# Optimization experiments

Measured on AMD Instinct MI355X. Metric: run time of the kernel, lower is better.

## Reference

```python
import jax, jax.numpy as jnp
import numpy as np

HEADS = 16
EPS = 1e-6


def setup_inputs() -> dict:
    key = jax.random.key(0)
    k1, k2, k3 = jax.random.split(key, 3)
    B, N, C = 4, 4096, 1024
    x = jax.random.normal(k1, (B, N, C), dtype=jnp.float32)
    w_qkv = jax.random.normal(k2, (3 * C, C), dtype=jnp.float32) * (C ** -0.5)
    w_out = jax.random.normal(k3, (C, C), dtype=jnp.float32) * (C ** -0.5)
    b_out = jnp.zeros((C,), dtype=jnp.float32)
    return {"x": x, "w_qkv": w_qkv, "w_out": w_out, "b_out": b_out}


def reference(x, w_qkv, w_out, b_out):
    B, N, C = x.shape
    H = HEADS
    D = C // H
    scale = D ** -0.25

    qkv = x @ w_qkv.T  # [B, N, 3C]
    q, k, v = jnp.split(qkv, 3, axis=-1)

    def heads(t):  # [B, N, C] -> [B, H, N, D]
        return t.reshape(B, N, H, D).transpose(0, 2, 1, 3)

    q, k, v = heads(q), heads(k), heads(v)

    feat = lambda t: jax.nn.elu(t) + 1.0
    q = feat(q) * scale
    k = feat(k) * scale

    kv = jnp.einsum('bhnd,bhne->bhde', k, v)      # [B, H, D, D]
    out = jnp.einsum('bhnd,bhde->bhne', q, kv)    # [B, H, N, D]
    k_sum = k.sum(axis=2)                          # [B, H, D]
    denom = jnp.einsum('bhnd,bhd->bhn', q, k_sum)  # [B, H, N]
    out = out / (denom[..., None] + EPS)

    out = out.transpose(0, 2, 1, 3).reshape(B, N, C)
    return out @ w_out.T + b_out
```

## Files before the change

kernel.cpp:

```cpp
#include <hip/hip_runtime.h>
#include <hip/hip_bf16.h>
#include <cmath>


typedef __bf16 bf16_t;
typedef __attribute__((ext_vector_type(8))) __bf16 bf16x8;
typedef __attribute__((ext_vector_type(4))) __bf16 bf16x4;
typedef __attribute__((ext_vector_type(4))) float f32x4;
typedef __attribute__((ext_vector_type(8))) float f32x8;

#define MFMA16(a, b, c) __builtin_amdgcn_mfma_f32_16x16x32_bf16((a), (b), (c), 0, 0, 0)

#define LDS_PITCH 72

__device__ __forceinline__ f32x4 zf4() { f32x4 z; z[0] = 0.f; z[1] = 0.f; z[2] = 0.f; z[3] = 0.f; return z; }

__device__ __forceinline__ float feat(float x) { return x > 0.f ? x + 1.f : expf(x); }

__device__ __forceinline__ void gld_lds16(const bf16_t* src, bf16_t* dst)
{
    __builtin_amdgcn_global_load_lds(
        (__attribute__((address_space(1))) void*)const_cast<bf16_t*>(src),
        (__attribute__((address_space(3))) void*)dst, 16, 0, 0);
}

template <int NR>
__device__ __forceinline__ void stage_async(const bf16_t* g, int ld, bf16_t* lds, int tid)
{
    const int w = tid >> 6, l = tid & 63;
    constexpr int CALLS = NR >> 5;
#pragma unroll
    for (int p = 0; p < CALLS; ++p) {
        const int chunk = w * CALLS + p;
        const int gidx = chunk * 64 + l;
        const int row = gidx >> 3;
        const int cp = gidx & 7;
        const int c = cp ^ (row & 7);
        gld_lds16(g + row * ld + c * 8, lds + chunk * 512);
    }
}

__device__ __forceinline__ bf16x8 read_frag_sw(const bf16_t* lds, int row, int cg)
{
    const int sw = cg ^ (row & 7);
    return *(const bf16x8*)(lds + row * 64 + sw * 8);
}

template <int NR>
__device__ __forceinline__ void stage_bf16(const bf16_t* g, int ld, bf16_t* lds, int tid)
{
#pragma unroll
    for (int p = 0; p < NR * 8 / 256; ++p) {
        const int gidx = p * 256 + tid;
        const int row = gidx >> 3;
        const int cp = gidx & 7;
        *(bf16x8*)(lds + row * LDS_PITCH + cp * 8) = *(const bf16x8*)(g + row * ld + cp * 8);
    }
}

__device__ __forceinline__ bf16x8 read_frag(const bf16_t* lds, int row, int cg)
{
    return *(const bf16x8*)(lds + row * LDS_PITCH + cg * 8);
}

__global__ __launch_bounds__(256) void cvt_kernel(const float* __restrict__ src, bf16_t* __restrict__ dst)
{
    const size_t idx = ((size_t)blockIdx.x * 256 + threadIdx.x) * 8;
    f32x8 f = *(const f32x8*)(src + idx);
    bf16x8 v;
#pragma unroll
    for (int t = 0; t < 8; ++t) v[t] = (bf16_t)f[t];
    *(bf16x8*)(dst + idx) = v;
}

template <int MODE>
__global__ __launch_bounds__(256, 3) void gemm_bt_kernel(
    const bf16_t* __restrict__ A, const bf16_t* __restrict__ B, int K,
    void* __restrict__ out0, bf16_t* __restrict__ out1, bf16_t* __restrict__ out2,
    const float* __restrict__ bias)
{
    __shared__ __align__(16) bf16_t As[128 * 64];
    __shared__ __align__(16) bf16_t Bs[128 * 64];
    const int tid = threadIdx.x;
    const int l = tid & 63, w = tid >> 6;
    const int wm = w >> 1, wn = w & 1;
    const int quad = l >> 4, r16 = l & 15;
    const int m0 = blockIdx.y * 128;
    const int n0 = blockIdx.x * 128;

    f32x4 acc[4][4];
#pragma unroll
    for (int i = 0; i < 4; ++i)
#pragma unroll
        for (int j = 0; j < 4; ++j) acc[i][j] = zf4();

    const bf16_t* Ab = A + (size_t)m0 * K;
    const bf16_t* Bb = B + (size_t)n0 * K;

    for (int k0 = 0; k0 < K; k0 += 64) {
        stage_async<128>(Ab + k0, K, As, tid);
        stage_async<128>(Bb + k0, K, Bs, tid);
        __syncthreads();
#pragma unroll
        for (int ks = 0; ks < 2; ++ks) {
            const int cg = ks * 4 + quad;
            bf16x8 af[4], bfr[4];
#pragma unroll
            for (int i = 0; i < 4; ++i) af[i] = read_frag_sw(As, wm * 64 + i * 16 + r16, cg);
#pragma unroll
            for (int j = 0; j < 4; ++j) bfr[j] = read_frag_sw(Bs, wn * 64 + j * 16 + r16, cg);
#pragma unroll
            for (int i = 0; i < 4; ++i)
#pragma unroll
                for (int j = 0; j < 4; ++j)
                    acc[i][j] = MFMA16(af[i], bfr[j], acc[i][j]);
        }
        __syncthreads();
    }

    const float scale = 0.3535533905932738f;
#pragma unroll
    for (int i = 0; i < 4; ++i) {
        const int mbase = m0 + wm * 64 + i * 16 + quad * 4;
#pragma unroll
        for (int j = 0; j < 4; ++j) {
            const int col = n0 + wn * 64 + j * 16 + r16;
            if (MODE == 1) {
                float* yp = (float*)out0;
                const float bb = bias[col];
#pragma unroll
                for (int r = 0; r < 4; ++r)
                    yp[(size_t)(mbase + r) * 1024 + col] = acc[i][j][r] + bb;
            } else {
                const int part = col >> 10;
                const int cc = col & 1023;
                const int hh = (mbase >> 12) * 16 + (cc >> 6);
                const int d = cc & 63;
                const int ntok = mbase & 4095;
                if (part == 0) {
                    bf16_t* qp = (bf16_t*)out0 + ((size_t)hh * 4096 + ntok) * 64 + d;
#pragma unroll
                    for (int r = 0; r < 4; ++r)
                        qp[(size_t)r * 64] = (bf16_t)(feat(acc[i][j][r]) * scale);
                } else {
                    bf16_t* tp = (part == 1 ? out1 : out2) + ((size_t)hh * 64 + d) * 4096 + ntok;
                    bf16x4 pk;
#pragma unroll
                    for (int r = 0; r < 4; ++r) {
                        float v = acc[i][j][r];
                        if (part == 1) v = feat(v) * scale;
                        pk[r] = (bf16_t)v;
                    }
                    *(bf16x4*)tp = pk;
                }
            }
        }
    }
}

__global__ __launch_bounds__(256, 2) void kv_partial_kernel(
    const bf16_t* __restrict__ KT, const bf16_t* __restrict__ VT,
    float* __restrict__ kvp, float* __restrict__ ksp_out)
{
    __shared__ __align__(16) bf16_t Ks[64 * LDS_PITCH];
    __shared__ __align__(16) bf16_t Vs[64 * LDS_PITCH];
    const int tid = threadIdx.x;
    const int l = tid & 63, w = tid >> 6;
    const int quad = l >> 4, r16 = l & 15;
    const int hh = blockIdx.x;
    const int ksp = blockIdx.y;
    const bf16_t* kb = KT + (size_t)hh * 64 * 4096 + ksp * 1024;
    const bf16_t* vb = VT + (size_t)hh * 64 * 4096 + ksp * 1024;

    bf16x8 ones;
#pragma unroll
    for (int t = 0; t < 8; ++t) ones[t] = (bf16_t)1.0f;

    f32x4 acc[4], accks[4];
#pragma unroll
    for (int j = 0; j < 4; ++j) { acc[j] = zf4(); accks[j] = zf4(); }

    for (int k0 = 0; k0 < 1024; k0 += 64) {
        stage_bf16<64>(kb + k0, 4096, Ks, tid);
        stage_bf16<64>(vb + k0, 4096, Vs, tid);
        __syncthreads();
#pragma unroll
        for (int ks = 0; ks < 2; ++ks) {
            const int cg = ks * 4 + quad;
            bf16x8 af = read_frag(Vs, w * 16 + r16, cg);
            bf16x8 bk[4];
#pragma unroll
            for (int j = 0; j < 4; ++j) bk[j] = read_frag(Ks, j * 16 + r16, cg);
#pragma unroll
            for (int j = 0; j < 4; ++j) acc[j] = MFMA16(af, bk[j], acc[j]);
            if (w == 0) {
#pragma unroll
                for (int j = 0; j < 4; ++j) accks[j] = MFMA16(ones, bk[j], accks[j]);
            }
        }
        __syncthreads();
    }

    float* ob = kvp + (size_t)(hh * 4 + ksp) * 4096;
    const int ebase = w * 16 + quad * 4;
#pragma unroll
    for (int j = 0; j < 4; ++j)
#pragma unroll
        for (int r = 0; r < 4; ++r)
            ob[(ebase + r) * 64 + j * 16 + r16] = acc[j][r];

    if (w == 0 && quad == 0) {
        float* kso = ksp_out + (size_t)(hh * 4 + ksp) * 64;
#pragma unroll
        for (int j = 0; j < 4; ++j) kso[j * 16 + r16] = accks[j][0];
    }
}

__global__ __launch_bounds__(256) void kvfix_kernel(
    const float* __restrict__ kvp, const float* __restrict__ ksp,
    bf16_t* __restrict__ kvb, bf16_t* __restrict__ ksumb)
{
    const int hh = blockIdx.x, t = threadIdx.x;
    const float* base = kvp + (size_t)hh * 4 * 4096;
    const int off = t * 16;
    bf16x8 o[2];
#pragma unroll
    for (int c = 0; c < 4; ++c) {
        f32x4 s = *(const f32x4*)(base + off + c * 4);
        s += *(const f32x4*)(base + 4096 + off + c * 4);
        s += *(const f32x4*)(base + 8192 + off + c * 4);
        s += *(const f32x4*)(base + 12288 + off + c * 4);
#pragma unroll
        for (int r = 0; r < 4; ++r) o[c >> 1][(c & 1) * 4 + r] = (bf16_t)s[r];
    }
    *(bf16x8*)(kvb + (size_t)hh * 4096 + off) = o[0];
    *(bf16x8*)(kvb + (size_t)hh * 4096 + off + 8) = o[1];
    if (t < 64) {
        const float* kb = ksp + (size_t)hh * 4 * 64;
        ksumb[(size_t)hh * 64 + t] = (bf16_t)(kb[t] + kb[64 + t] + kb[128 + t] + kb[192 + t]);
    }
}

__global__ __launch_bounds__(256, 2) void attn_out_kernel(
    const bf16_t* __restrict__ Q, const bf16_t* __restrict__ kvb, const bf16_t* __restrict__ ksumb,
    bf16_t* __restrict__ att)
{
    __shared__ __align__(16) bf16_t kvT[64 * LDS_PITCH];
    __shared__ __align__(16) bf16_t ksb[64];
    const int tid = threadIdx.x;
    const int l = tid & 63, w = tid >> 6;
    const int quad = l >> 4, r16 = l & 15;
    const int hh = blockIdx.x;
    const int b = hh >> 4, h = hh & 15;
    const int mt = blockIdx.y;

    {
        const int e = tid >> 2, d0 = (tid & 3) * 16;
        const bf16_t* kvbh = kvb + (size_t)hh * 4096;
        *(bf16x8*)(kvT + e * LDS_PITCH + d0)     = *(const bf16x8*)(kvbh + e * 64 + d0);
        *(bf16x8*)(kvT + e * LDS_PITCH + d0 + 8) = *(const bf16x8*)(kvbh + e * 64 + d0 + 8);
        if (tid < 64) ksb[tid] = ksumb[(size_t)hh * 64 + tid];
    }
    __syncthreads();

    f32x4 acc[4][4];
    f32x4 dacc[4];
#pragma unroll
    for (int i = 0; i < 4; ++i) {
        dacc[i] = zf4();
#pragma unroll
        for (int j = 0; j < 4; ++j) acc[i][j] = zf4();
    }

    const int m0w = mt * 256 + w * 64;
    const bf16_t* qb = Q + (size_t)hh * 4096 * 64;
#pragma unroll
    for (int ks = 0; ks < 2; ++ks) {
        bf16x8 kf = *(const bf16x8*)(ksb + ks * 32 + quad * 8);
        if (r16 != 0) {
#pragma unroll
            for (int t = 0; t < 8; ++t) kf[t] = (bf16_t)0.f;
        }
        bf16x8 bfr[4];
#pragma unroll
        for (int j = 0; j < 4; ++j)
            bfr[j] = *(const bf16x8*)(kvT + (j * 16 + r16) * LDS_PITCH + ks * 32 + quad * 8);
#pragma unroll
        for (int i = 0; i < 4; ++i) {
            const bf16_t* qp = qb + (size_t)(m0w + i * 16 + r16) * 64 + ks * 32 + quad * 8;
            const bf16x8 af = *(const bf16x8*)qp;
            dacc[i] = MFMA16(af, kf, dacc[i]);
#pragma unroll
            for (int j = 0; j < 4; ++j) acc[i][j] = MFMA16(af, bfr[j], acc[i][j]);
        }
    }

#pragma unroll
    for (int i = 0; i < 4; ++i) {
        float den[4];
#pragma unroll
        for (int r = 0; r < 4; ++r)
            den[r] = __shfl(dacc[i][r], l & 48) + 1e-6f;
#pragma unroll
        for (int j = 0; j < 4; ++j) {
            const size_t colb = (size_t)h * 64 + j * 16 + r16;
#pragma unroll
            for (int r = 0; r < 4; ++r) {
                const int ntok = m0w + i * 16 + quad * 4 + r;
                att[((size_t)b * 4096 + ntok) * 1024 + colb] = (bf16_t)(acc[i][j][r] / den[r]);
            }
        }
    }
}

extern "C" void kernel_launch(void* const* d_in, const int* in_sizes, int n_in,
                              void* d_out, int out_size, void* d_ws, size_t ws_size,
                              hipStream_t stream)
{
    const float* x    = (const float*)d_in[0];
    const float* wqkv = (const float*)d_in[1];
    const float* wout = (const float*)d_in[2];
    const float* bout = (const float*)d_in[3];
    float* y = (float*)d_out;

    char* ws = (char*)d_ws;
    bf16_t* xb    = (bf16_t*)ws;
    bf16_t* wqkvb = (bf16_t*)(ws + (size_t)32 * 1048576);
    bf16_t* woutb = (bf16_t*)(ws + (size_t)38 * 1048576);
    bf16_t* Q     = (bf16_t*)(ws + (size_t)40 * 1048576);
    bf16_t* KT    = (bf16_t*)(ws + (size_t)72 * 1048576);
    bf16_t* VT    = (bf16_t*)(ws + (size_t)104 * 1048576);
    float* kvp    = (float*)ws;
    float* ksp    = (float*)(ws + (size_t)4 * 1048576);
    bf16_t* kvb   = (bf16_t*)(ws + (size_t)5 * 1048576);
    bf16_t* ksumb = (bf16_t*)(ws + (size_t)6 * 1048576);
    bf16_t* att   = KT;

    cvt_kernel<<<8192, 256, 0, stream>>>(x, xb);
    cvt_kernel<<<1536, 256, 0, stream>>>(wqkv, wqkvb);
    cvt_kernel<<<512, 256, 0, stream>>>(wout, woutb);

    gemm_bt_kernel<0><<<dim3(24, 128), 256, 0, stream>>>(xb, wqkvb, 1024, Q, KT, VT, nullptr);
    kv_partial_kernel<<<dim3(64, 4), 256, 0, stream>>>(KT, VT, kvp, ksp);
    kvfix_kernel<<<64, 256, 0, stream>>>(kvp, ksp, kvb, ksumb);
    attn_out_kernel<<<dim3(64, 16), 256, 0, stream>>>(Q, kvb, ksumb, att);
    gemm_bt_kernel<1><<<dim3(8, 128), 256, 0, stream>>>(att, woutb, 1024, y, nullptr, nullptr, bout);
}
```

Before: 332.6 us.

## Use 256x256 tiles with double-buffered async LDS pipeline in GEMM kernel

Both GEMMs move from a 128x128 tile with 4 waves to a 256x256 tile with 8 waves and 128 KB of double-buffered LDS. Global-to-LDS async loads for future K-tiles are split into regions and issued between MFMA phases, with explicit vmcnt waits, barriers and setprio so loads overlap compute. The aim is more data reuse per block and hiding memory latency. In exchange it uses more registers and LDS, allows fewer blocks per CU, and launches fewer blocks (256 for the output GEMM), so the last wave of blocks may leave CUs idle.

```diff
diff --git a/kernel.cpp b/kernel.cpp
--- a/kernel.cpp
+++ b/kernel.cpp
@@ -24,26 +24,31 @@
         (__attribute__((address_space(3))) void*)dst, 16, 0, 0);
 }
 
-template <int NR>
-__device__ __forceinline__ void stage_async(const bf16_t* g, int ld, bf16_t* lds, int tid)
+template <int R>
+__device__ __forceinline__ void stage_region(const bf16_t* Ab, const bf16_t* Bb, int K,
+                                             int koff, bf16_t* buf, int tid)
 {
     const int w = tid >> 6, l = tid & 63;
-    constexpr int CALLS = NR >> 5;
-#pragma unroll
-    for (int p = 0; p < CALLS; ++p) {
-        const int chunk = w * CALLS + p;
+    bf16_t* dst = buf + R * 8192;
+#pragma unroll
+    for (int p = 0; p < 2; ++p) {
+        const int chunk = w * 2 + p;
         const int gidx = chunk * 64 + l;
-        const int row = gidx >> 3;
-        const int cp = gidx & 7;
-        const int c = cp ^ (row & 7);
-        gld_lds16(g + row * ld + c * 8, lds + chunk * 512);
-    }
-}
-
-__device__ __forceinline__ bf16x8 read_frag_sw(const bf16_t* lds, int row, int cg)
-{
-    const int sw = cg ^ (row & 7);
-    return *(const bf16x8*)(lds + row * 64 + sw * 8);
+        const int rr = gidx >> 3;
+        const int c = (gidx & 7) ^ (rr & 7);
+        const bf16_t* src;
+        if (R == 0)      src = Bb + (size_t)rr * K;
+        else if (R == 1) src = Bb + (size_t)(128 + rr) * K;
+        else if (R == 2) src = Ab + (size_t)(rr + (rr & 64)) * K;
+        else             src = Ab + (size_t)(64 + rr + (rr & 64)) * K;
+        gld_lds16(src + koff + c * 8, dst + chunk * 512);
+    }
+}
+
+__device__ __forceinline__ bf16x8 rfrag(const bf16_t* region, int rr, int cg)
+{
+    const int sw = cg ^ (rr & 7);
+    return *(const bf16x8*)(region + rr * 64 + sw * 8);
 }
 
 template <int NR>
@@ -74,54 +79,118 @@
 }
 
 template <int MODE>
-__global__ __launch_bounds__(256, 3) void gemm_bt_kernel(
+__global__ __launch_bounds__(512, 2) void gemm_bt_kernel(
     const bf16_t* __restrict__ A, const bf16_t* __restrict__ B, int K,
     void* __restrict__ out0, bf16_t* __restrict__ out1, bf16_t* __restrict__ out2,
     const float* __restrict__ bias)
 {
-    __shared__ __align__(16) bf16_t As[128 * 64];
-    __shared__ __align__(16) bf16_t Bs[128 * 64];
+    __shared__ __align__(16) bf16_t lds[2 * 32768];
     const int tid = threadIdx.x;
     const int l = tid & 63, w = tid >> 6;
-    const int wm = w >> 1, wn = w & 1;
+    const int wm = w >> 2, wn = w & 3;
     const int quad = l >> 4, r16 = l & 15;
-    const int m0 = blockIdx.y * 128;
-    const int n0 = blockIdx.x * 128;
-
-    f32x4 acc[4][4];
-#pragma unroll
-    for (int i = 0; i < 4; ++i)
-#pragma unroll
-        for (int j = 0; j < 4; ++j) acc[i][j] = zf4();
+    const int m0 = blockIdx.y * 256;
+    const int n0 = blockIdx.x * 256;
+    const int NT = K >> 6;
 
     const bf16_t* Ab = A + (size_t)m0 * K;
     const bf16_t* Bb = B + (size_t)n0 * K;
 
-    for (int k0 = 0; k0 < K; k0 += 64) {
-        stage_async<128>(Ab + k0, K, As, tid);
-        stage_async<128>(Bb + k0, K, Bs, tid);
-        __syncthreads();
-#pragma unroll
-        for (int ks = 0; ks < 2; ++ks) {
-            const int cg = ks * 4 + quad;
-            bf16x8 af[4], bfr[4];
-#pragma unroll
-            for (int i = 0; i < 4; ++i) af[i] = read_frag_sw(As, wm * 64 + i * 16 + r16, cg);
-#pragma unroll
-            for (int j = 0; j < 4; ++j) bfr[j] = read_frag_sw(Bs, wn * 64 + j * 16 + r16, cg);
-#pragma unroll
-            for (int i = 0; i < 4; ++i)
+    f32x4 acc[8][4];
+#pragma unroll
+    for (int i = 0; i < 8; ++i)
+#pragma unroll
+        for (int j = 0; j < 4; ++j) acc[i][j] = zf4();
+
+    stage_region<0>(Ab, Bb, K, 0, lds, tid);
+    stage_region<1>(Ab, Bb, K, 0, lds, tid);
+    stage_region<2>(Ab, Bb, K, 0, lds, tid);
+    stage_region<3>(Ab, Bb, K, 0, lds, tid);
+    stage_region<0>(Ab, Bb, K, 64, lds + 32768, tid);
+    stage_region<1>(Ab, Bb, K, 64, lds + 32768, tid);
+    stage_region<2>(Ab, Bb, K, 64, lds + 32768, tid);
+    asm volatile("s_waitcnt vmcnt(6)" ::: "memory");
+    __builtin_amdgcn_sched_barrier(0);
+    __builtin_amdgcn_s_barrier();
+
+    for (int t = 0; t < NT; ++t) {
+        bf16_t* cb = lds + (t & 1) * 32768;
+        bf16_t* nb = lds + ((t & 1) ^ 1) * 32768;
+
+        bf16x8 bfr[4][2], af[2][2];
+
+        const bf16_t* breg = cb + (wn >> 1) * 8192;
+#pragma unroll
+        for (int j = 0; j < 4; ++j) {
+            const int rr = (wn & 1) * 64 + j * 16 + r16;
+            bfr[j][0] = rfrag(breg, rr, quad);
+            bfr[j][1] = rfrag(breg, rr, 4 + quad);
+        }
+#pragma unroll
+        for (int i2 = 0; i2 < 2; ++i2) {
+            const int rr = wm * 64 + i2 * 16 + r16;
+            af[i2][0] = rfrag(cb + 2 * 8192, rr, quad);
+            af[i2][1] = rfrag(cb + 2 * 8192, rr, 4 + quad);
+        }
+        if (t + 1 < NT) stage_region<3>(Ab, Bb, K, (t + 1) * 64, nb, tid);
+        __builtin_amdgcn_s_barrier();
+        asm volatile("s_waitcnt lgkmcnt(0)" ::: "memory");
+        __builtin_amdgcn_sched_barrier(0);
+        __builtin_amdgcn_s_setprio(1);
+#pragma unroll
+        for (int ks = 0; ks < 2; ++ks)
+#pragma unroll
+            for (int i2 = 0; i2 < 2; ++i2)
 #pragma unroll
                 for (int j = 0; j < 4; ++j)
-                    acc[i][j] = MFMA16(af[i], bfr[j], acc[i][j]);
-        }
-        __syncthreads();
+                    acc[i2][j] = MFMA16(af[i2][ks], bfr[j][ks], acc[i2][j]);
+        __builtin_amdgcn_s_setprio(0);
+        __builtin_amdgcn_s_barrier();
+
+#pragma unroll
+        for (int ph = 1; ph < 4; ++ph) {
+            const int mb = ph * 2;
+#pragma unroll
+            for (int i2 = 0; i2 < 2; ++i2) {
+                const int i = mb + i2;
+                const bf16_t* areg = cb + (size_t)(2 + (i >> 2)) * 8192;
+                const int rr = wm * 64 + (i & 3) * 16 + r16;
+                af[i2][0] = rfrag(areg, rr, quad);
+                af[i2][1] = rfrag(areg, rr, 4 + quad);
+            }
+            if (t + 2 < NT) {
+                if (ph == 1) stage_region<0>(Ab, Bb, K, (t + 2) * 64, cb, tid);
+                if (ph == 2) stage_region<1>(Ab, Bb, K, (t + 2) * 64, cb, tid);
+                if (ph == 3) stage_region<2>(Ab, Bb, K, (t + 2) * 64, cb, tid);
+            }
+            if (ph == 3) {
+                if (t + 2 < NT) {
+                    asm volatile("s_waitcnt vmcnt(6)" ::: "memory");
+                } else if (t + 2 == NT) {
+                    asm volatile("s_waitcnt vmcnt(0)" ::: "memory");
+                }
+                __builtin_amdgcn_sched_barrier(0);
+            }
+            __builtin_amdgcn_s_barrier();
+            asm volatile("s_waitcnt lgkmcnt(0)" ::: "memory");
+            __builtin_amdgcn_sched_barrier(0);
+            __builtin_amdgcn_s_setprio(1);
+#pragma unroll
+            for (int ks = 0; ks < 2; ++ks)
+#pragma unroll
+                for (int i2 = 0; i2 < 2; ++i2)
+#pragma unroll
+                    for (int j = 0; j < 4; ++j)
+                        acc[mb + i2][j] = MFMA16(af[i2][ks], bfr[j][ks], acc[mb + i2][j]);
+            __builtin_amdgcn_s_setprio(0);
+            __builtin_amdgcn_s_barrier();
+        }
     }
 
     const float scale = 0.3535533905932738f;
 #pragma unroll
-    for (int i = 0; i < 4; ++i) {
-        const int mbase = m0 + wm * 64 + i * 16 + quad * 4;
+    for (int i = 0; i < 8; ++i) {
+        const int mbase = m0 + wm * 128 + i * 16 + quad * 4;
 #pragma unroll
         for (int j = 0; j < 4; ++j) {
             const int col = n0 + wn * 64 + j * 16 + r16;
@@ -340,9 +409,9 @@
     cvt_kernel<<<1536, 256, 0, stream>>>(wqkv, wqkvb);
     cvt_kernel<<<512, 256, 0, stream>>>(wout, woutb);
 
-    gemm_bt_kernel<0><<<dim3(24, 128), 256, 0, stream>>>(xb, wqkvb, 1024, Q, KT, VT, nullptr);
+    gemm_bt_kernel<0><<<dim3(12, 64), 512, 0, stream>>>(xb, wqkvb, 1024, Q, KT, VT, nullptr);
     kv_partial_kernel<<<dim3(64, 4), 256, 0, stream>>>(KT, VT, kvp, ksp);
     kvfix_kernel<<<64, 256, 0, stream>>>(kvp, ksp, kvb, ksumb);
     attn_out_kernel<<<dim3(64, 16), 256, 0, stream>>>(Q, kvb, ksumb, att);
-    gemm_bt_kernel<1><<<dim3(8, 128), 256, 0, stream>>>(att, woutb, 1024, y, nullptr, nullptr, bout);
-}
+    gemm_bt_kernel<1><<<dim3(4, 64), 512, 0, stream>>>(att, woutb, 1024, y, nullptr, nullptr, bout);
+}
```

After: 333.2 us. No clear change (+0.2%).

## Rewrite GEMM as 256x256 tile, 8-wave, double-buffered ping-pong pipeline

Applied to the files above, without the earlier changes.

Replaces the 128x128, 4-wave GEMM with a 256x256 tile computed by 8 waves. Each wave now owns 128x64 of output. K-panels are double-buffered in LDS through async global-to-LDS loads, with fine-grained vmcnt waits, barriers and s_setprio so loads overlap the MFMA bursts. The aim is more data reuse per loaded byte and hidden global latency. In exchange it uses 128KB of LDS, more accumulator registers per wave, and fewer blocks: 768 and 256 tiles across 256 CUs.

```diff
diff --git a/kernel.cpp b/kernel.cpp
--- a/kernel.cpp
+++ b/kernel.cpp
@@ -24,26 +24,34 @@
         (__attribute__((address_space(3))) void*)dst, 16, 0, 0);
 }
 
-template <int NR>
-__device__ __forceinline__ void stage_async(const bf16_t* g, int ld, bf16_t* lds, int tid)
+template <int RT>
+__device__ __forceinline__ const bf16_t* panel_src(const bf16_t* Ab, const bf16_t* Bb, int K, int rr)
+{
+    if (RT == 0) return Bb + (size_t)rr * K;
+    if (RT == 1) return Bb + (size_t)(128 + rr) * K;
+    if (RT == 2) return Ab + (size_t)(rr + (rr & 64)) * K;
+    return Ab + (size_t)(64 + rr + (rr & 64)) * K;
+}
+
+template <int RT>
+__device__ __forceinline__ void stage_panel(const bf16_t* Ab, const bf16_t* Bb, int K,
+                                            int koff, bf16_t* dst, int tid)
 {
     const int w = tid >> 6, l = tid & 63;
-    constexpr int CALLS = NR >> 5;
-#pragma unroll
-    for (int p = 0; p < CALLS; ++p) {
-        const int chunk = w * CALLS + p;
+#pragma unroll
+    for (int p = 0; p < 2; ++p) {
+        const int chunk = w * 2 + p;
         const int gidx = chunk * 64 + l;
-        const int row = gidx >> 3;
-        const int cp = gidx & 7;
-        const int c = cp ^ (row & 7);
-        gld_lds16(g + row * ld + c * 8, lds + chunk * 512);
-    }
-}
-
-__device__ __forceinline__ bf16x8 read_frag_sw(const bf16_t* lds, int row, int cg)
-{
-    const int sw = cg ^ (row & 7);
-    return *(const bf16x8*)(lds + row * 64 + sw * 8);
+        const int rr = gidx >> 3;
+        const int c = (gidx & 7) ^ (rr & 7);
+        gld_lds16(panel_src<RT>(Ab, Bb, K, rr) + koff + c * 8, dst + chunk * 512);
+    }
+}
+
+__device__ __forceinline__ bf16x8 rfrag(const bf16_t* panel, int rr, int cg)
+{
+    const int sw = cg ^ (rr & 7);
+    return *(const bf16x8*)(panel + rr * 64 + sw * 8);
 }
 
 template <int NR>
@@ -73,55 +81,117 @@
     *(bf16x8*)(dst + idx) = v;
 }
 
+#define GBAR() __builtin_amdgcn_s_barrier()
+#define WAITL() do { asm volatile("s_waitcnt lgkmcnt(0)" ::: "memory"); \
+                     __builtin_amdgcn_sched_barrier(0); } while (0)
+#define VMC6() do { asm volatile("s_waitcnt vmcnt(6)" ::: "memory"); \
+                    __builtin_amdgcn_sched_barrier(0); } while (0)
+#define VMC0() do { asm volatile("s_waitcnt vmcnt(0)" ::: "memory"); \
+                    __builtin_amdgcn_sched_barrier(0); } while (0)
+
 template <int MODE>
-__global__ __launch_bounds__(256, 3) void gemm_bt_kernel(
+__global__ __launch_bounds__(512, 2) void gemm_bt_kernel(
     const bf16_t* __restrict__ A, const bf16_t* __restrict__ B, int K,
     void* __restrict__ out0, bf16_t* __restrict__ out1, bf16_t* __restrict__ out2,
     const float* __restrict__ bias)
 {
-    __shared__ __align__(16) bf16_t As[128 * 64];
-    __shared__ __align__(16) bf16_t Bs[128 * 64];
+    __shared__ __align__(16) bf16_t B0a[8192], B0b[8192], A0a[8192], A0b[8192];
+    __shared__ __align__(16) bf16_t B1a[8192], B1b[8192], A1a[8192], A1b[8192];
     const int tid = threadIdx.x;
     const int l = tid & 63, w = tid >> 6;
-    const int wm = w >> 1, wn = w & 1;
+    const int wm = w >> 2, wn = w & 3;
     const int quad = l >> 4, r16 = l & 15;
-    const int m0 = blockIdx.y * 128;
-    const int n0 = blockIdx.x * 128;
-
-    f32x4 acc[4][4];
-#pragma unroll
-    for (int i = 0; i < 4; ++i)
-#pragma unroll
-        for (int j = 0; j < 4; ++j) acc[i][j] = zf4();
+    const int m0 = blockIdx.y * 256;
+    const int n0 = blockIdx.x * 256;
+    const int NT = K >> 6;
 
     const bf16_t* Ab = A + (size_t)m0 * K;
     const bf16_t* Bb = B + (size_t)n0 * K;
 
-    for (int k0 = 0; k0 < K; k0 += 64) {
-        stage_async<128>(Ab + k0, K, As, tid);
-        stage_async<128>(Bb + k0, K, Bs, tid);
-        __syncthreads();
-#pragma unroll
-        for (int ks = 0; ks < 2; ++ks) {
-            const int cg = ks * 4 + quad;
-            bf16x8 af[4], bfr[4];
-#pragma unroll
-            for (int i = 0; i < 4; ++i) af[i] = read_frag_sw(As, wm * 64 + i * 16 + r16, cg);
-#pragma unroll
-            for (int j = 0; j < 4; ++j) bfr[j] = read_frag_sw(Bs, wn * 64 + j * 16 + r16, cg);
-#pragma unroll
-            for (int i = 0; i < 4; ++i)
+    f32x4 acc[8][4];
+#pragma unroll
+    for (int i = 0; i < 8; ++i)
+#pragma unroll
+        for (int j = 0; j < 4; ++j) acc[i][j] = zf4();
+
+    bf16x8 bfr[4][2], af[2][2];
+
+    auto loadB = [&](const bf16_t* Blo, const bf16_t* Bhi) {
+        const bf16_t* breg = (wn & 2) ? Bhi : Blo;
+#pragma unroll
+        for (int j = 0; j < 4; ++j) {
+            const int rr = (wn & 1) * 64 + j * 16 + r16;
+            bfr[j][0] = rfrag(breg, rr, quad);
+            bfr[j][1] = rfrag(breg, rr, 4 + quad);
+        }
+    };
+    auto loadA = [&](const bf16_t* areg, int fr) {
+#pragma unroll
+        for (int i2 = 0; i2 < 2; ++i2) {
+            const int rr = wm * 64 + (fr + i2) * 16 + r16;
+            af[i2][0] = rfrag(areg, rr, quad);
+            af[i2][1] = rfrag(areg, rr, 4 + quad);
+        }
+    };
+    auto mfma8 = [&](int mb) {
+        __builtin_amdgcn_s_setprio(1);
+#pragma unroll
+        for (int ks = 0; ks < 2; ++ks)
+#pragma unroll
+            for (int i2 = 0; i2 < 2; ++i2)
 #pragma unroll
                 for (int j = 0; j < 4; ++j)
-                    acc[i][j] = MFMA16(af[i], bfr[j], acc[i][j]);
-        }
-        __syncthreads();
+                    acc[mb + i2][j] = MFMA16(af[i2][ks], bfr[j][ks], acc[mb + i2][j]);
+        __builtin_amdgcn_s_setprio(0);
+    };
+
+    stage_panel<0>(Ab, Bb, K, 0, B0a, tid);
+    stage_panel<1>(Ab, Bb, K, 0, B0b, tid);
+    stage_panel<2>(Ab, Bb, K, 0, A0a, tid);
+    stage_panel<3>(Ab, Bb, K, 0, A0b, tid);
+    stage_panel<0>(Ab, Bb, K, 64, B1a, tid);
+    stage_panel<1>(Ab, Bb, K, 64, B1b, tid);
+    stage_panel<2>(Ab, Bb, K, 64, A1a, tid);
+    VMC6();
+    GBAR();
+
+    for (int t = 0; t < NT; t += 2) {
+        const int k2 = (t + 2) * 64, k3 = (t + 3) * 64;
+        const bool p2 = (t + 2) < NT, p3 = (t + 3) < NT;
+
+        loadB(B0a, B0b); loadA(A0a, 0);
+        stage_panel<3>(Ab, Bb, K, (t + 1) * 64, A1b, tid);
+        GBAR(); WAITL(); mfma8(0); GBAR();
+        loadA(A0a, 2);
+        if (p2) stage_panel<0>(Ab, Bb, K, k2, B0a, tid);
+        GBAR(); WAITL(); mfma8(2); GBAR();
+        loadA(A0b, 0);
+        if (p2) stage_panel<1>(Ab, Bb, K, k2, B0b, tid);
+        GBAR(); WAITL(); mfma8(4); GBAR();
+        loadA(A0b, 2);
+        if (p2) { stage_panel<2>(Ab, Bb, K, k2, A0a, tid); VMC6(); }
+        else    { VMC0(); }
+        GBAR(); WAITL(); mfma8(6); GBAR();
+
+        loadB(B1a, B1b); loadA(A1a, 0);
+        if (p2) stage_panel<3>(Ab, Bb, K, k2, A0b, tid);
+        GBAR(); WAITL(); mfma8(0); GBAR();
+        loadA(A1a, 2);
+        if (p3) stage_panel<0>(Ab, Bb, K, k3, B1a, tid);
+        GBAR(); WAITL(); mfma8(2); GBAR();
+        loadA(A1b, 0);
+        if (p3) stage_panel<1>(Ab, Bb, K, k3, B1b, tid);
+        GBAR(); WAITL(); mfma8(4); GBAR();
+        loadA(A1b, 2);
+        if (p3) { stage_panel<2>(Ab, Bb, K, k3, A1a, tid); VMC6(); }
+        else    { VMC0(); }
+        GBAR(); WAITL(); mfma8(6); GBAR();
     }
 
     const float scale = 0.3535533905932738f;
 #pragma unroll
-    for (int i = 0; i < 4; ++i) {
-        const int mbase = m0 + wm * 64 + i * 16 + quad * 4;
+    for (int i = 0; i < 8; ++i) {
+        const int mbase = m0 + wm * 128 + i * 16 + quad * 4;
 #pragma unroll
         for (int j = 0; j < 4; ++j) {
             const int col = n0 + wn * 64 + j * 16 + r16;
@@ -340,9 +410,9 @@
     cvt_kernel<<<1536, 256, 0, stream>>>(wqkv, wqkvb);
     cvt_kernel<<<512, 256, 0, stream>>>(wout, woutb);
 
-    gemm_bt_kernel<0><<<dim3(24, 128), 256, 0, stream>>>(xb, wqkvb, 1024, Q, KT, VT, nullptr);
+    gemm_bt_kernel<0><<<dim3(12, 64), 512, 0, stream>>>(xb, wqkvb, 1024, Q, KT, VT, nullptr);
     kv_partial_kernel<<<dim3(64, 4), 256, 0, stream>>>(KT, VT, kvp, ksp);
     kvfix_kernel<<<64, 256, 0, stream>>>(kvp, ksp, kvb, ksumb);
     attn_out_kernel<<<dim3(64, 16), 256, 0, stream>>>(Q, kvb, ksumb, att);
-    gemm_bt_kernel<1><<<dim3(8, 128), 256, 0, stream>>>(att, woutb, 1024, y, nullptr, nullptr, bout);
-}
+    gemm_bt_kernel<1><<<dim3(4, 64), 512, 0, stream>>>(att, woutb, 1024, y, nullptr, nullptr, bout);
+}
```

Measured after the change: 324.8 us. 2.3% less time.
